# Performance work log

Measured on AMD Instinct MI355X. Metric: run time of the kernel, lower is better.

The kernel has to match this reference:

```python
import jax, jax.numpy as jnp
import numpy as np

NUM_SPECIES = 4
NUM_PAIRS = NUM_SPECIES * (NUM_SPECIES + 1) // 2  # 10 species pairs
RCR = 5.2   # radial cutoff (Angstrom)
RCA = 3.5   # angular cutoff (must be < RCR)
ETA_R = 16.0
SHF_R = jnp.asarray(0.9 + 0.26875 * np.arange(16), dtype=jnp.float32)
ETA_A = 8.0
ZETA = 32.0
SHF_A = jnp.asarray(0.9 + 0.65 * np.arange(4), dtype=jnp.float32)       # 4 angular radial shifts
SHF_Z = jnp.asarray((np.pi / 16.0) * (1.0 + 2.0 * np.arange(8)), dtype=jnp.float32)  # 8 angle sections


def _triu_index(num_species):
    # mirrors AEVComputer._calculate_triu_index
    s1, s2 = np.triu_indices(num_species, 0)
    ret = np.zeros((num_species, num_species), dtype=np.int32)
    ret[s1, s2] = np.arange(len(s1))
    ret[s2, s1] = np.arange(len(s1))
    return jnp.asarray(ret)

TRIU = _triu_index(NUM_SPECIES)


def _fc(d, rc):
    # cosine cutoff; the (d <= rc) validity is applied via masks outside
    return 0.5 * jnp.cos(jnp.pi * d / rc) + 0.5


def _aev(species, coords):
    N, A = species.shape
    dt = coords.dtype
    diff = coords[:, None, :, :] - coords[:, :, None, :]          # (N,i,j,3): r_j - r_i
    eye = jnp.eye(A, dtype=bool)
    d2 = jnp.sum(diff * diff, axis=-1)
    dist = jnp.sqrt(jnp.where(eye, 1.0, d2))                      # (N,i,j), self-distance guarded

    # ---- radial AEV: 0.25 * exp(-EtaR*(d-ShfR)^2) * fc(d), scattered by neighbor species ----
    rmask = (~eye) & (dist <= RCR)
    rad = 0.25 * jnp.exp(-ETA_R * (dist[..., None] - SHF_R) ** 2) * _fc(dist, RCR)[..., None]
    rad = rad * rmask[..., None].astype(dt)                       # (N,i,j,16)
    sp1h = jax.nn.one_hot(species, NUM_SPECIES, dtype=dt)         # (N,j,S)
    radial_aev = jnp.einsum('nijr,njs->nisr', rad, sp1h).reshape(N, A, -1)  # (N,A,64)

    # ---- angular AEV over triples (i; j,k), j,k neighbors of i within RCA ----
    amask = (~eye) & (dist <= RCA)                                # (N,i,j)
    tri = amask[:, :, :, None] & amask[:, :, None, :] & (~eye)[None, None]  # (N,i,j,k), j!=k
    dot = jnp.einsum('nijc,nikc->nijk', diff, diff)
    cos = 0.95 * dot / (dist[:, :, :, None] * dist[:, :, None, :])  # 0.95 stabilizer as in torchani
    theta = jnp.arccos(jnp.clip(cos, -0.95, 0.95))                # (N,i,j,k)
    fcj = _fc(dist, RCA)
    base = 2.0 * fcj[:, :, :, None] * fcj[:, :, None, :] * tri.astype(dt)
    davg = 0.5 * (dist[:, :, :, None] + dist[:, :, None, :])
    f2 = jnp.exp(-ETA_A * (davg[..., None] - SHF_A) ** 2)         # (N,i,j,k,ShfA=4)
    f1 = ((1.0 + jnp.cos(theta[..., None] - SHF_Z)) * 0.5) ** ZETA  # (N,i,j,k,ShfZ=8)
    term = (base[..., None, None] * f2[..., :, None] * f1[..., None, :]).reshape(N, A, A, A, -1)
    pair_idx = TRIU[species[:, :, None], species[:, None, :]]     # (N,j,k)
    pair1h = jax.nn.one_hot(pair_idx, NUM_PAIRS, dtype=dt)        # (N,j,k,P=10)
    # each unordered pair {j,k} is counted once in torchani -> 0.5 * symmetric ordered sum
    angular_aev = 0.5 * jnp.einsum('nijkq,njkp->nipq', term, pair1h).reshape(N, A, -1)  # (N,A,320)

    return jnp.concatenate([radial_aev, angular_aev], axis=-1)    # (N,A,384)


def setup_inputs():
    key = jax.random.key(0)
    k1, k2 = jax.random.split(key)
    N, A, BOX = 16, 64, 12.0
    coords = jax.random.uniform(k1, (N, A, 3), dtype=jnp.float32) * BOX  # atoms in a 12 A box
    species = jax.random.randint(k2, (N, A), 0, NUM_SPECIES)
    return {"species": species, "coords": coords}


def reference(species, coords):
    # SpeciesAEV: (species, aev) with aev shape (N, A, aev_length=384)
    return species, _aev(species, coords)
```

## Files before the change

kernel.cpp:

```cpp
#include <hip/hip_runtime.h>

#define RCR 5.2f
#define RCA 3.5f
#define PI_F 3.14159265358979323846f

__global__ __launch_bounds__(128) void aev_kernel(
    const int* __restrict__ species,
    const float* __restrict__ coords,
    float* __restrict__ out,
    int NA)
{
    const int blk  = blockIdx.x;
    const int n    = blk >> 6;
    const int i    = blk & 63;
    const int tid  = threadIdx.x;
    const int lane = tid & 63;
    const int wave = tid >> 6;

    __shared__ float sx[64], sy[64], sz[64];
    __shared__ int   ssp[64];
    __shared__ float adx[64], ady[64], adz[64], ads[64], afc[64];
    __shared__ int   asp[64];
    __shared__ float rds[4][65], rpre[4][65];
    __shared__ int   cnts[5];
    __shared__ float s_ang[320];

    if (tid < 64) {
        const float* c = coords + (size_t)(n * 64) * 3;
        sx[tid]  = c[tid * 3 + 0];
        sy[tid]  = c[tid * 3 + 1];
        sz[tid]  = c[tid * 3 + 2];
        ssp[tid] = species[n * 64 + tid];
    }
    for (int f = tid; f < 320; f += 128) s_ang[f] = 0.0f;
    __syncthreads();

    if (wave == 0) {
        const float xi  = sx[i], yi = sy[i], zi = sz[i];
        const float ddx = sx[lane] - xi;
        const float ddy = sy[lane] - yi;
        const float ddz = sz[lane] - zi;
        const float d   = sqrtf(ddx * ddx + ddy * ddy + ddz * ddz);
        const bool  isj = (lane != i);
        const int   sp  = ssp[lane];
        const float pre = 0.25f * (0.5f * __cosf((PI_F / RCR) * d) + 0.5f);
        const float fcv = 0.5f * __cosf((PI_F / RCA) * d) + 0.5f;

        const bool rpred = isj && (d <= RCR);
        #pragma unroll
        for (int s = 0; s < 4; s++) {
            const bool p = rpred && (sp == s);
            const unsigned long long b = __ballot(p);
            if (p) {
                const int pos = __popcll(b & ((1ull << lane) - 1ull));
                rds[s][pos]  = d;
                rpre[s][pos] = pre;
            }
            if (lane == 0) cnts[s] = __popcll(b);
        }

        const bool apred = isj && (d <= RCA);
        const unsigned long long b = __ballot(apred);
        if (apred) {
            const int pos = __popcll(b & ((1ull << lane) - 1ull));
            adx[pos] = ddx; ady[pos] = ddy; adz[pos] = ddz;
            ads[pos] = d;   afc[pos] = fcv; asp[pos] = sp;
        }
        if (lane == 0) cnts[4] = __popcll(b);
    }
    __syncthreads();

    float racc = 0.0f;
    if (wave == 0) {
        const int   s   = lane >> 4;
        const float shf = 0.9f + 0.26875f * (float)(lane & 15);
        const int   mr  = cnts[s];
        #pragma unroll 4
        for (int jj = 0; jj < mr; jj++) {
            const float t = rds[s][jj] - shf;
            racc += rpre[s][jj] * __expf(-16.0f * t * t);
        }
    } else {
        const float CPHI[8] = { 0.98078528f,  0.83146961f,  0.55557023f,  0.19509032f,
                               -0.19509032f, -0.55557023f, -0.83146961f, -0.98078528f};
        const float SPHI[8] = { 0.19509032f,  0.55557023f,  0.83146961f,  0.98078528f,
                                0.98078528f,  0.83146961f,  0.55557023f,  0.19509032f};
        const float SHFA[4] = {0.9f, 1.55f, 2.2f, 2.85f};

        const int M = cnts[4];
        const int P = (M * (M - 1)) >> 1;
        for (int q = lane; q < P; q += 64) {
            int jj = (int)((1.0f + sqrtf(1.0f + 8.0f * (float)q)) * 0.5f);
            while (((jj * (jj - 1)) >> 1) > q) --jj;
            while ((((jj + 1) * jj) >> 1) <= q) ++jj;
            const int kk = q - ((jj * (jj - 1)) >> 1);

            const float dij = ads[jj], dik = ads[kk];
            const float dot = adx[jj] * adx[kk] + ady[jj] * ady[kk] + adz[jj] * adz[kk];
            float cosv = 0.95f * dot * __builtin_amdgcn_rcpf(dij * dik);
            cosv = fminf(0.95f, fmaxf(-0.95f, cosv));
            const float sinv  = sqrtf(fmaxf(0.0f, 1.0f - cosv * cosv));
            const float base2 = 2.0f * afc[jj] * afc[kk];
            const float davg  = 0.5f * (dij + dik);
            const int s1 = asp[jj], s2 = asp[kk];
            const int smin = (s1 < s2) ? s1 : s2;
            const int smax = (s1 < s2) ? s2 : s1;
            const int pidx = ((smin * (7 - smin)) >> 1) + smax;

            float f2[4];
            #pragma unroll
            for (int a = 0; a < 4; a++) {
                const float t = davg - SHFA[a];
                f2[a] = base2 * __expf(-8.0f * t * t);
            }
            float t32z[8];
            #pragma unroll
            for (int z = 0; z < 8; z++) {
                const float w  = 0.5f + 0.5f * (cosv * CPHI[z] + sinv * SPHI[z]);
                const float t2 = w * w, t4 = t2 * t2, t8 = t4 * t4, t16 = t8 * t8;
                t32z[z] = t16 * t16;
            }
            float* dst = &s_ang[pidx * 32];
            #pragma unroll
            for (int a = 0; a < 4; a++)
                #pragma unroll
                for (int z = 0; z < 8; z++)
                    atomicAdd(&dst[a * 8 + z], f2[a] * t32z[z]);
        }
    }
    __syncthreads();

    const int atom = n * 64 + i;
    if (tid == 0) out[atom] = (float)ssp[i];
    float* dstg = out + NA + (size_t)atom * 384;
    if (wave == 0) dstg[lane] = racc;
    for (int u = tid; u < 320; u += 128) dstg[64 + u] = s_ang[u];
}

extern "C" void kernel_launch(void* const* d_in, const int* in_sizes, int n_in,
                              void* d_out, int out_size, void* d_ws, size_t ws_size,
                              hipStream_t stream) {
    const int*   species = (const int*)d_in[0];
    const float* coords  = (const float*)d_in[1];
    float*       out     = (float*)d_out;
    const int NA = in_sizes[0];
    aev_kernel<<<NA, 128, 0, stream>>>(species, coords, out, NA);
}
```

Baseline: 62.15 us.

## Replicate angular accumulators and split each pair's angle sections across two lanes

Result: no change. 62.29 us (+0.2%).

```diff
diff --git a/kernel.cpp b/kernel.cpp
--- a/kernel.cpp
+++ b/kernel.cpp
@@ -23,16 +23,17 @@
     __shared__ int   asp[64];
     __shared__ float rds[4][65], rpre[4][65];
     __shared__ int   cnts[5];
-    __shared__ float s_ang[320];
+    __shared__ float s_ang[4 * 328];
 
     if (tid < 64) {
         const float* c = coords + (size_t)(n * 64) * 3;
         sx[tid]  = c[tid * 3 + 0];
         sy[tid]  = c[tid * 3 + 1];
         sz[tid]  = c[tid * 3 + 2];
-        ssp[tid] = species[n * 64 + tid];
+    } else {
+        ssp[lane] = species[n * 64 + lane];
     }
-    for (int f = tid; f < 320; f += 128) s_ang[f] = 0.0f;
+    for (int f = tid; f < 4 * 328; f += 128) s_ang[f] = 0.0f;
     __syncthreads();
 
     if (wave == 0) {
@@ -70,16 +71,21 @@
     }
     __syncthreads();
 
-    float racc = 0.0f;
+    const int atom = n * 64 + i;
+    float* dstg = out + NA + (size_t)atom * 384;
+
     if (wave == 0) {
         const int   s   = lane >> 4;
         const float shf = 0.9f + 0.26875f * (float)(lane & 15);
         const int   mr  = cnts[s];
+        float racc = 0.0f;
         #pragma unroll 4
         for (int jj = 0; jj < mr; jj++) {
             const float t = rds[s][jj] - shf;
             racc += rpre[s][jj] * __expf(-16.0f * t * t);
         }
+        dstg[lane] = racc;
+        if (lane == 0) out[atom] = (float)ssp[i];
     } else {
         const float CPHI[8] = { 0.98078528f,  0.83146961f,  0.55557023f,  0.19509032f,
                                -0.19509032f, -0.55557023f, -0.83146961f, -0.98078528f};
@@ -88,8 +94,10 @@
         const float SHFA[4] = {0.9f, 1.55f, 2.2f, 2.85f};
 
         const int M = cnts[4];
-        const int P = (M * (M - 1)) >> 1;
-        for (int q = lane; q < P; q += 64) {
+        const int W = (M * (M - 1));
+        for (int idx = lane; idx < W; idx += 64) {
+            const int q = idx >> 1;
+            const int g = idx & 1;
             int jj = (int)((1.0f + sqrtf(1.0f + 8.0f * (float)q)) * 0.5f);
             while (((jj * (jj - 1)) >> 1) > q) --jj;
             while ((((jj + 1) * jj) >> 1) <= q) ++jj;
@@ -113,28 +121,33 @@
                 const float t = davg - SHFA[a];
                 f2[a] = base2 * __expf(-8.0f * t * t);
             }
-            float t32z[8];
+            float t32z[4];
             #pragma unroll
-            for (int z = 0; z < 8; z++) {
+            for (int z4 = 0; z4 < 4; z4++) {
+                const int z = 4 * g + z4;
                 const float w  = 0.5f + 0.5f * (cosv * CPHI[z] + sinv * SPHI[z]);
                 const float t2 = w * w, t4 = t2 * t2, t8 = t4 * t4, t16 = t8 * t8;
-                t32z[z] = t16 * t16;
+                t32z[z4] = t16 * t16;
             }
-            float* dst = &s_ang[pidx * 32];
+            float* dst = &s_ang[(lane & 3) * 328 + pidx * 32];
+            const int arot = lane & 3, zrot = (lane >> 2) & 3;
             #pragma unroll
-            for (int a = 0; a < 4; a++)
+            for (int aa = 0; aa < 4; aa++) {
+                const int a = (aa + arot) & 3;
                 #pragma unroll
-                for (int z = 0; z < 8; z++)
-                    atomicAdd(&dst[a * 8 + z], f2[a] * t32z[z]);
+                for (int zz = 0; zz < 4; zz++) {
+                    const int z4 = (zz + zrot) & 3;
+                    atomicAdd(&dst[a * 8 + 4 * g + z4], f2[a] * t32z[z4]);
+                }
+            }
         }
     }
     __syncthreads();
 
-    const int atom = n * 64 + i;
-    if (tid == 0) out[atom] = (float)ssp[i];
-    float* dstg = out + NA + (size_t)atom * 384;
-    if (wave == 0) dstg[lane] = racc;
-    for (int u = tid; u < 320; u += 128) dstg[64 + u] = s_ang[u];
+    for (int u = tid; u < 320; u += 128) {
+        dstg[64 + u] = (s_ang[u] + s_ang[328 + u])
+                     + (s_ang[656 + u] + s_ang[984 + u]);
+    }
 }
 
 extern "C" void kernel_launch(void* const* d_in, const int* in_sizes, int n_in,
```
